# Performance work log

Hardware: AMD Instinct MI355X
Metric: run time of the kernel (lower is better)

## Reference

```python
import jax, jax.numpy as jnp
import numpy as np

N, D = 16384, 128
T = 0.07  # temperature


def setup_inputs() -> dict:
    key = jax.random.key(0)
    x = jax.random.normal(key, (N, D), dtype=jnp.float32)
    # uniformity loss assumes unit-norm embeddings (else exp(||x||^2 / t) overflows)
    x = x / jnp.linalg.norm(x, axis=-1, keepdims=True)
    return {"x": x}


def reference(x):
    # x.matmul(x.T).div(t).exp().sum(-1).log().mean()
    sims = jnp.matmul(x, x.T) / T            # [N, N]
    return jnp.mean(jnp.log(jnp.sum(jnp.exp(sims), axis=-1)))
```

## Files before the change

kernel.cpp:

```cpp
#include <hip/hip_runtime.h>
#include <hip/hip_bf16.h>

#define NN 16384
#define DD 128
#define BM 128
#define BCOLS 4096
#define TILES 32
#define NBLOCKS 512
#define SQRT_SCALE 4.5398159622f

typedef __attribute__((ext_vector_type(8))) short bf16x8;
typedef __attribute__((ext_vector_type(4))) float f32x4;

__global__ void convert_swz(const float* __restrict__ x, ushort* __restrict__ xb) {
    int t = blockIdx.x * blockDim.x + threadIdx.x;
    int r = t >> 4;
    int c = t & 15;
    const float4* src = (const float4*)(x + (size_t)r * DD + c * 8);
    float4 f0 = src[0];
    float4 f1 = src[1];
    float vals[8] = {f0.x, f0.y, f0.z, f0.w, f1.x, f1.y, f1.z, f1.w};
    bf16x8 v;
#pragma unroll
    for (int i = 0; i < 8; ++i) {
        __hip_bfloat16 h = __float2bfloat16(vals[i] * SQRT_SCALE);
        v[i] = (short)__builtin_bit_cast(unsigned short, h);
    }
    int cs = c ^ (r & 15);
    *(bf16x8*)(xb + (size_t)r * DD + cs * 8) = v;
}

__global__ __launch_bounds__(512, 4) void gemm_exp_stream(const ushort* __restrict__ xb,
                                                          float* __restrict__ rowsumP) {
    __shared__ __align__(16) ushort lB[2][128 * DD];
    __shared__ float xch[4][32];

    const int tid  = threadIdx.x;
    const int lane = tid & 63;
    const int wid  = tid >> 6;
    const int frow = lane & 15;
    const int kq   = lane >> 4;

    const int bid    = blockIdx.x;
    const int cq     = (bid & 7) >> 1;
    const int rstrip = ((bid >> 3) << 1) | (bid & 1);
    const int rw = wid >> 1;
    const int cw = wid & 1;
    const int R0 = rstrip * BM;
    const int C0 = cq * BCOLS;

    auto stage = [&](int buf, int t) {
        const char* g = (const char*)(xb + (size_t)(C0 + t * 128) * DD);
#pragma unroll
        for (int i = 0; i < 4; ++i) {
            int off = (wid * 4 + i) * 1024;
            __builtin_amdgcn_global_load_lds(
                (const __attribute__((address_space(1))) unsigned int*)(g + off + lane * 16),
                (__attribute__((address_space(3))) unsigned int*)((char*)&lB[buf][0] + off),
                16, 0, 0);
        }
    };

    stage(0, 0);

    bf16x8 af[2][4];
#pragma unroll
    for (int m = 0; m < 2; ++m)
#pragma unroll
        for (int kk = 0; kk < 4; ++kk) {
            int ra = R0 + rw * 32 + m * 16 + frow;
            int slot = (kk * 4 + kq) ^ frow;
            af[m][kk] = *(const bf16x8*)(xb + (size_t)ra * DD + slot * 8);
        }

    int nbase[4], kkoff[4];
#pragma unroll
    for (int n = 0; n < 4; ++n)
        nbase[n] = (cw * 64 + n * 16 + frow) * 256 + ((kq ^ (frow & 3)) << 4);
#pragma unroll
    for (int kk = 0; kk < 4; ++kk)
        kkoff[kk] = (((kk << 2) ^ (frow & 12)) << 4);

    const f32x4 zacc = {0.f, 0.f, 0.f, 0.f};
    float rs[2][4] = {};

    for (int t = 0; t < TILES; ++t) {
        const int cur = t & 1;
        if (t < TILES - 1) {
            stage(cur ^ 1, t + 1);
            asm volatile("s_waitcnt vmcnt(4)" ::: "memory");
        } else {
            asm volatile("s_waitcnt vmcnt(0)" ::: "memory");
        }
        __builtin_amdgcn_s_barrier();

        const char* Bb = (const char*)&lB[cur][0];
        f32x4 acc[2][4];
#pragma unroll
        for (int kk = 0; kk < 4; ++kk) {
            bf16x8 bfr[4];
#pragma unroll
            for (int n = 0; n < 4; ++n)
                bfr[n] = *(const bf16x8*)(Bb + nbase[n] + kkoff[kk]);
            __builtin_amdgcn_s_setprio(1);
            if (kk == 0) {
#pragma unroll
                for (int m = 0; m < 2; ++m)
#pragma unroll
                    for (int n = 0; n < 4; ++n)
                        acc[m][n] = __builtin_amdgcn_mfma_f32_16x16x32_bf16(
                            af[m][0], bfr[n], zacc, 0, 0, 0);
            } else {
#pragma unroll
                for (int m = 0; m < 2; ++m)
#pragma unroll
                    for (int n = 0; n < 4; ++n)
                        acc[m][n] = __builtin_amdgcn_mfma_f32_16x16x32_bf16(
                            af[m][kk], bfr[n], acc[m][n], 0, 0, 0);
            }
            __builtin_amdgcn_s_setprio(0);
        }
        __builtin_amdgcn_s_barrier();

#pragma unroll
        for (int m = 0; m < 2; ++m)
#pragma unroll
            for (int j = 0; j < 4; ++j) {
                float s = (__builtin_amdgcn_exp2f(acc[m][0][j]) +
                           __builtin_amdgcn_exp2f(acc[m][1][j])) +
                          (__builtin_amdgcn_exp2f(acc[m][2][j]) +
                           __builtin_amdgcn_exp2f(acc[m][3][j]));
                rs[m][j] += s;
            }
    }

#pragma unroll
    for (int m = 0; m < 2; ++m)
#pragma unroll
        for (int j = 0; j < 4; ++j) {
            float s = rs[m][j];
            s += __shfl_xor(s, 1);
            s += __shfl_xor(s, 2);
            s += __shfl_xor(s, 4);
            s += __shfl_xor(s, 8);
            rs[m][j] = s;
        }

    if (frow == 0 && cw == 1) {
#pragma unroll
        for (int m = 0; m < 2; ++m)
#pragma unroll
            for (int j = 0; j < 4; ++j)
                xch[rw][m * 16 + kq * 4 + j] = rs[m][j];
    }
    __syncthreads();
    if (frow == 0 && cw == 0) {
        float* dst = rowsumP + (size_t)cq * NN + R0 + rw * 32 + kq * 4;
#pragma unroll
        for (int m = 0; m < 2; ++m) {
            float4 v = {rs[m][0] + xch[rw][m * 16 + kq * 4 + 0],
                        rs[m][1] + xch[rw][m * 16 + kq * 4 + 1],
                        rs[m][2] + xch[rw][m * 16 + kq * 4 + 2],
                        rs[m][3] + xch[rw][m * 16 + kq * 4 + 3]};
            *(float4*)(dst + m * 16) = v;
        }
    }
}

__global__ void finalize_part(const float* __restrict__ rowsumP,
                              float* __restrict__ partial) {
    const int tid = threadIdx.x;
    const int r = blockIdx.x * 256 + tid;
    float rsum = 0.f;
#pragma unroll
    for (int p = 0; p < 4; ++p)
        rsum += rowsumP[p * NN + r];
    float s = __builtin_amdgcn_logf(rsum) * 0.69314718056f;
#pragma unroll
    for (int o = 1; o < 64; o <<= 1)
        s += __shfl_xor(s, o);
    __shared__ float wsum[4];
    if ((tid & 63) == 0) wsum[tid >> 6] = s;
    __syncthreads();
    if (tid == 0)
        partial[blockIdx.x] = wsum[0] + wsum[1] + wsum[2] + wsum[3];
}

__global__ void finalize_sum(const float* __restrict__ partial, float* __restrict__ out) {
    float s = partial[threadIdx.x];
#pragma unroll
    for (int o = 1; o < 64; o <<= 1)
        s += __shfl_xor(s, o);
    if (threadIdx.x == 0)
        out[0] = s * (1.0f / NN);
}

extern "C" void kernel_launch(void* const* d_in, const int* in_sizes, int n_in,
                              void* d_out, int out_size, void* d_ws, size_t ws_size,
                              hipStream_t stream) {
    const float* x = (const float*)d_in[0];
    float* out = (float*)d_out;

    ushort* xb     = (ushort*)d_ws;
    float* rowsumP = (float*)((char*)d_ws + (size_t)NN * DD * 2);
    float* partial = rowsumP + 4 * NN;

    convert_swz<<<(NN * 16) / 256, 256, 0, stream>>>(x, xb);
    gemm_exp_stream<<<NBLOCKS, 512, 0, stream>>>(xb, rowsumP);
    finalize_part<<<64, 256, 0, stream>>>(rowsumP, partial);
    finalize_sum<<<1, 64, 0, stream>>>(partial, out);
}
```

Measured before the change: 83.07 us.

## Exploit Gram matrix symmetry with triangular tiling and bit-trick exp

```diff
diff --git a/kernel.cpp b/kernel.cpp
--- a/kernel.cpp
+++ b/kernel.cpp
@@ -3,14 +3,17 @@
 
 #define NN 16384
 #define DD 128
-#define BM 128
-#define BCOLS 4096
-#define TILES 32
-#define NBLOCKS 512
+#define NSTRIP 128
+#define NRANK 16512
 #define SQRT_SCALE 4.5398159622f
+
+#define EXP_A 8388608.0f
+#define EXP_K 1064986316.0f
 
 typedef __attribute__((ext_vector_type(8))) short bf16x8;
 typedef __attribute__((ext_vector_type(4))) float f32x4;
+
+#define RANK0(s) ((s) * (257 - (s)))
 
 __global__ void convert_swz(const float* __restrict__ x, ushort* __restrict__ xb) {
     int t = blockIdx.x * blockDim.x + threadIdx.x;
@@ -30,10 +33,10 @@
     *(bf16x8*)(xb + (size_t)r * DD + cs * 8) = v;
 }
 
-__global__ __launch_bounds__(512, 4) void gemm_exp_stream(const ushort* __restrict__ xb,
-                                                          float* __restrict__ rowsumP) {
-    __shared__ __align__(16) ushort lB[2][128 * DD];
-    __shared__ float xch[4][32];
+__global__ __launch_bounds__(256, 3) void gemm_exp_tri(const ushort* __restrict__ xb,
+                                                       float* __restrict__ rowsum,
+                                                       ushort* __restrict__ colscr) {
+    __shared__ __align__(16) ushort lB[2][64 * DD];
 
     const int tid  = threadIdx.x;
     const int lane = tid & 63;
@@ -41,16 +44,20 @@
     const int frow = lane & 15;
     const int kq   = lane >> 4;
 
-    const int bid    = blockIdx.x;
-    const int cq     = (bid & 7) >> 1;
-    const int rstrip = ((bid >> 3) << 1) | (bid & 1);
-    const int rw = wid >> 1;
-    const int cw = wid & 1;
-    const int R0 = rstrip * BM;
-    const int C0 = cq * BCOLS;
-
-    auto stage = [&](int buf, int t) {
-        const char* g = (const char*)(xb + (size_t)(C0 + t * 128) * DD);
+    const int bid = blockIdx.x;
+    const int s   = bid >> 4;
+    const int k   = bid & 15;
+    const int c0  = 2 * s + k;
+    if (c0 > 255) return;
+    const int nt  = ((255 - c0) >> 4) + 1;
+
+    int slot[4];
+#pragma unroll
+    for (int kk = 0; kk < 4; ++kk)
+        slot[kk] = ((((kk << 2) | kq) ^ frow) << 3);
+
+    auto stage = [&](int buf, int c) {
+        const char* g = (const char*)(xb + (size_t)c * 64 * DD);
 #pragma unroll
         for (int i = 0; i < 4; ++i) {
             int off = (wid * 4 + i) * 1024;
@@ -61,48 +68,45 @@
         }
     };
 
-    stage(0, 0);
+    stage(0, c0);
 
     bf16x8 af[2][4];
 #pragma unroll
-    for (int m = 0; m < 2; ++m)
-#pragma unroll
-        for (int kk = 0; kk < 4; ++kk) {
-            int ra = R0 + rw * 32 + m * 16 + frow;
-            int slot = (kk * 4 + kq) ^ frow;
-            af[m][kk] = *(const bf16x8*)(xb + (size_t)ra * DD + slot * 8);
-        }
+    for (int m = 0; m < 2; ++m) {
+        const ushort* p = xb + (size_t)(s * 128 + wid * 32 + m * 16 + frow) * DD;
+#pragma unroll
+        for (int kk = 0; kk < 4; ++kk)
+            af[m][kk] = *(const bf16x8*)(p + slot[kk]);
+    }
 
     int nbase[4], kkoff[4];
 #pragma unroll
     for (int n = 0; n < 4; ++n)
-        nbase[n] = (cw * 64 + n * 16 + frow) * 256 + ((kq ^ (frow & 3)) << 4);
+        nbase[n] = (n * 16 + frow) * 256;
 #pragma unroll
     for (int kk = 0; kk < 4; ++kk)
-        kkoff[kk] = (((kk << 2) ^ (frow & 12)) << 4);
+        kkoff[kk] = slot[kk] * 2;
+
+    asm volatile("s_waitcnt vmcnt(0)" ::: "memory");
+    __builtin_amdgcn_s_barrier();
 
     const f32x4 zacc = {0.f, 0.f, 0.f, 0.f};
     float rs[2][4] = {};
-
-    for (int t = 0; t < TILES; ++t) {
-        const int cur = t & 1;
-        if (t < TILES - 1) {
-            stage(cur ^ 1, t + 1);
-            asm volatile("s_waitcnt vmcnt(4)" ::: "memory");
-        } else {
-            asm volatile("s_waitcnt vmcnt(0)" ::: "memory");
-        }
-        __builtin_amdgcn_s_barrier();
+    const int rank0 = RANK0(s) + k;
+
+    for (int q = 0; q < nt; ++q) {
+        const int cur = q & 1;
+        if (q + 1 < nt) stage(cur ^ 1, c0 + 16 * (q + 1));
 
         const char* Bb = (const char*)&lB[cur][0];
         f32x4 acc[2][4];
+        __builtin_amdgcn_s_setprio(1);
 #pragma unroll
         for (int kk = 0; kk < 4; ++kk) {
             bf16x8 bfr[4];
 #pragma unroll
             for (int n = 0; n < 4; ++n)
                 bfr[n] = *(const bf16x8*)(Bb + nbase[n] + kkoff[kk]);
-            __builtin_amdgcn_s_setprio(1);
             if (kk == 0) {
 #pragma unroll
                 for (int m = 0; m < 2; ++m)
@@ -118,80 +122,104 @@
                         acc[m][n] = __builtin_amdgcn_mfma_f32_16x16x32_bf16(
                             af[m][kk], bfr[n], acc[m][n], 0, 0, 0);
             }
-            __builtin_amdgcn_s_setprio(0);
-        }
+        }
+        __builtin_amdgcn_s_setprio(0);
+
+        float cs[4] = {0.f, 0.f, 0.f, 0.f};
+#pragma unroll
+        for (int m = 0; m < 2; ++m)
+#pragma unroll
+            for (int n = 0; n < 4; ++n)
+#pragma unroll
+                for (int j = 0; j < 4; ++j) {
+                    float b = __builtin_fmaf(acc[m][n][j], EXP_A, EXP_K);
+                    float e = __builtin_bit_cast(float, (int)b);
+                    rs[m][j] += e;
+                    cs[n] += e;
+                }
+#pragma unroll
+        for (int n = 0; n < 4; ++n) {
+            float v = cs[n];
+            v += __shfl_xor(v, 16);
+            v += __shfl_xor(v, 32);
+            cs[n] = v;
+        }
+        const bool diag = (q == 0) && (k < 2);
+        if (kq == 0) {
+            const int rank = rank0 + 16 * q;
+            size_t base = ((size_t)rank * 4 + wid) * 64 + frow;
+#pragma unroll
+            for (int n = 0; n < 4; ++n) {
+                ushort v = diag ? (ushort)0
+                         : __builtin_bit_cast(ushort, __float2bfloat16(cs[n]));
+                colscr[base + n * 16] = v;
+            }
+        }
+
+        asm volatile("s_waitcnt vmcnt(0)" ::: "memory");
         __builtin_amdgcn_s_barrier();
-
+    }
+
+#pragma unroll
+    for (int m = 0; m < 2; ++m)
+#pragma unroll
+        for (int j = 0; j < 4; ++j) {
+            float v = rs[m][j];
+            v += __shfl_xor(v, 1);
+            v += __shfl_xor(v, 2);
+            v += __shfl_xor(v, 4);
+            v += __shfl_xor(v, 8);
+            rs[m][j] = v;
+        }
+    if (frow == 0) {
 #pragma unroll
         for (int m = 0; m < 2; ++m)
 #pragma unroll
-            for (int j = 0; j < 4; ++j) {
-                float s = (__builtin_amdgcn_exp2f(acc[m][0][j]) +
-                           __builtin_amdgcn_exp2f(acc[m][1][j])) +
-                          (__builtin_amdgcn_exp2f(acc[m][2][j]) +
-                           __builtin_amdgcn_exp2f(acc[m][3][j]));
-                rs[m][j] += s;
-            }
-    }
-
-#pragma unroll
-    for (int m = 0; m < 2; ++m)
-#pragma unroll
-        for (int j = 0; j < 4; ++j) {
-            float s = rs[m][j];
-            s += __shfl_xor(s, 1);
-            s += __shfl_xor(s, 2);
-            s += __shfl_xor(s, 4);
-            s += __shfl_xor(s, 8);
-            rs[m][j] = s;
-        }
-
-    if (frow == 0 && cw == 1) {
-#pragma unroll
-        for (int m = 0; m < 2; ++m)
-#pragma unroll
             for (int j = 0; j < 4; ++j)
-                xch[rw][m * 16 + kq * 4 + j] = rs[m][j];
-    }
+                atomicAdd(&rowsum[s * 128 + wid * 32 + m * 16 + kq * 4 + j],
+                          rs[m][j]);
+    }
+}
+
+__global__ __launch_bounds__(256) void colfin(const ushort* __restrict__ colscr,
+                                              const float* __restrict__ rowsum,
+                                              float* __restrict__ partial) {
+    const int c = blockIdx.x;
+    const int t = threadIdx.x;
+    const int e = t & 63;
+    const int w = t >> 6;
+    const int smax = c >> 1;
+
+    float a = 0.f;
+    for (int s = 0; s <= smax; ++s) {
+        int rank = RANK0(s) + (c - 2 * s);
+        a += __bfloat162float(__builtin_bit_cast(__hip_bfloat16,
+                 colscr[((size_t)rank * 4 + w) * 64 + e]));
+    }
+    __shared__ float p[4][64];
+    p[w][e] = a;
     __syncthreads();
-    if (frow == 0 && cw == 0) {
-        float* dst = rowsumP + (size_t)cq * NN + R0 + rw * 32 + kq * 4;
-#pragma unroll
-        for (int m = 0; m < 2; ++m) {
-            float4 v = {rs[m][0] + xch[rw][m * 16 + kq * 4 + 0],
-                        rs[m][1] + xch[rw][m * 16 + kq * 4 + 1],
-                        rs[m][2] + xch[rw][m * 16 + kq * 4 + 2],
-                        rs[m][3] + xch[rw][m * 16 + kq * 4 + 3]};
-            *(float4*)(dst + m * 16) = v;
-        }
-    }
-}
-
-__global__ void finalize_part(const float* __restrict__ rowsumP,
-                              float* __restrict__ partial) {
-    const int tid = threadIdx.x;
-    const int r = blockIdx.x * 256 + tid;
-    float rsum = 0.f;
-#pragma unroll
-    for (int p = 0; p < 4; ++p)
-        rsum += rowsumP[p * NN + r];
-    float s = __builtin_amdgcn_logf(rsum) * 0.69314718056f;
+
+    float l = 0.f;
+    if (t < 64) {
+        float tot = p[0][t] + p[1][t] + p[2][t] + p[3][t];
+        float r = rowsum[c * 64 + t] + tot;
+        l = __builtin_amdgcn_logf(r) * 0.69314718056f;
+    }
+#pragma unroll
+    for (int o = 1; o < 64; o <<= 1)
+        l += __shfl_xor(l, o);
+    if (t == 0)
+        partial[c] = l;
+}
+
+__global__ void finalize_sum(const float* __restrict__ partial, float* __restrict__ out) {
+    const int t = threadIdx.x;
+    float s = (partial[t] + partial[t + 64]) + (partial[t + 128] + partial[t + 192]);
 #pragma unroll
     for (int o = 1; o < 64; o <<= 1)
         s += __shfl_xor(s, o);
-    __shared__ float wsum[4];
-    if ((tid & 63) == 0) wsum[tid >> 6] = s;
-    __syncthreads();
-    if (tid == 0)
-        partial[blockIdx.x] = wsum[0] + wsum[1] + wsum[2] + wsum[3];
-}
-
-__global__ void finalize_sum(const float* __restrict__ partial, float* __restrict__ out) {
-    float s = partial[threadIdx.x];
-#pragma unroll
-    for (int o = 1; o < 64; o <<= 1)
-        s += __shfl_xor(s, o);
-    if (threadIdx.x == 0)
+    if (t == 0)
         out[0] = s * (1.0f / NN);
 }
 
@@ -201,12 +229,14 @@
     const float* x = (const float*)d_in[0];
     float* out = (float*)d_out;
 
-    ushort* xb     = (ushort*)d_ws;
-    float* rowsumP = (float*)((char*)d_ws + (size_t)NN * DD * 2);
-    float* partial = rowsumP + 4 * NN;
-
+    ushort* xb      = (ushort*)d_ws;
+    float* rowsum   = (float*)((char*)d_ws + (size_t)NN * DD * 2);
+    float* partial  = rowsum + NN;
+    ushort* colscr  = (ushort*)(partial + 256);
+
+    hipMemsetAsync(rowsum, 0, NN * sizeof(float), stream);
     convert_swz<<<(NN * 16) / 256, 256, 0, stream>>>(x, xb);
-    gemm_exp_stream<<<NBLOCKS, 512, 0, stream>>>(xb, rowsumP);
-    finalize_part<<<64, 256, 0, stream>>>(rowsumP, partial);
+    gemm_exp_tri<<<NSTRIP * 16, 256, 0, stream>>>(xb, rowsum, colscr);
+    colfin<<<256, 256, 0, stream>>>(colscr, rowsum, partial);
     finalize_sum<<<1, 64, 0, stream>>>(partial, out);
 }
```

Result: slower. 96.46 us (+16.1%).
